# Optimization experiments

Hardware: AMD Instinct MI355X
Metric: run time of the kernel (lower is better)

The kernel has to match this reference:

```python
import jax, jax.numpy as jnp
import numpy as np
import math

B_, M_, T_, E_ = 4, 4, 128, 512
S_ = M_ * T_
H_ = 2048
NE, NS, TOPK, NHEAD = 8, 2, 2, 4
P_, GRUH, AK, AV = 128, 128, 64, 64


def _ln(x, s, b, eps=1e-5):
    mu = x.mean(-1, keepdims=True)
    var = x.var(-1, keepdims=True)
    return (x - mu) / jnp.sqrt(var + eps) * s + b


def _gru(x, Wih, bih, Whh, bhh):
    # x: [N, T, D] -> [N, T, GRUH]; torch nn.GRU cell equations
    Hh = Whh.shape[1]
    def step(h, xt):
        gi = xt @ Wih.T + bih
        gh = h @ Whh.T + bhh
        ir, iz, inn = jnp.split(gi, 3, axis=-1)
        hr, hz, hn = jnp.split(gh, 3, axis=-1)
        r = jax.nn.sigmoid(ir + hr)
        z = jax.nn.sigmoid(iz + hz)
        n = jnp.tanh(inn + r * hn)
        h = (1.0 - z) * n + z * h
        return h, h
    h0 = jnp.zeros((x.shape[0], Hh), x.dtype)
    _, hs = jax.lax.scan(step, h0, jnp.swapaxes(x, 0, 1))
    return jnp.swapaxes(hs, 0, 1)


def _router_logits(x4, rU, rR, rS, Wtp, btp, Wq, bq, Wk, bk, Wv, bv,
                   gWih, gbih, gWhh, gbhh, mW1, mb1, mW2, mb2):
    B, M, T, E = x4.shape
    proc = jax.nn.relu(x4 @ Wtp + btp)                  # [B,M,T,P]
    q = proc @ Wq + bq                                   # [B,M,T,AK]
    Rp = jnp.transpose(rR, (0, 3, 1, 2))                 # [B,T,M,M]
    Sp = jnp.transpose(rS, (0, 3, 1, 2))
    others = np.array([[j for j in range(M) if j != m] for m in range(M)])  # [M,M-1]
    mi = np.arange(M)[:, None]
    feat = jnp.stack([Rp[:, :, mi, others], Sp[:, :, mi, others]], axis=-1)  # [B,T,M,M-1,2]
    keys = feat @ Wk + bk                                # [B,T,M,M-1,AK]
    vals = feat @ Wv + bv                                # [B,T,M,M-1,AV]
    sc = jnp.einsum('bmtk,btmok->bmto', q, keys) / math.sqrt(AK)
    ctx = jnp.einsum('bmto,btmov->bmtv', jax.nn.softmax(sc, -1), vals)  # [B,M,T,AV]
    gin = jnp.concatenate([rU[..., None], ctx], -1).reshape(B * M, T, 1 + AV)
    hs = _gru(gin, gWih, gbih, gWhh, gbhh).reshape(B, M, T, GRUH)
    comb = jnp.concatenate([proc, hs], -1)               # [B,M,T,P+GRUH]
    return jax.nn.relu(comb @ mW1 + mb1) @ mW2 + mb2     # [B,M,T,NE]


def _forward(x, rU, rR, rS, M, T, Wtp, btp, Wq, bq, Wk, bk, Wv, bv,
             gWih, gbih, gWhh, gbhh, mW1, mb1, mW2, mb2,
             sWq, sbq, sWk, sbk, sWv, sbv, sWo, sbo, sln1s, sln1b,
             sW1, sb1, sW2, sb2, sln2s, sln2b, fW1, fb1, fW2, fb2):
    B, S, E = x.shape
    x4 = x.reshape(B, M, T, E)
    logits = _router_logits(x4, rU, rR, rS, Wtp, btp, Wq, bq, Wk, bk, Wv, bv,
                            gWih, gbih, gWhh, gbhh, mW1, mb1, mW2, mb2)
    NT = B * S
    lf = logits.reshape(NT, NE)
    probs = jax.nn.softmax(lf, -1)
    vals, idx = jax.lax.top_k(lf, TOPK)
    tw = jax.nn.softmax(vals, -1)                        # renormalized top-k weights
    tok = x.reshape(NT, E)
    out = jnp.zeros((NT, E), x.dtype)
    hd = E // NHEAD
    for e in range(NE):
        w = jnp.sum(jnp.where(idx == e, tw, 0.0), -1)    # [NT] per-token weight for expert e
        if e < NS:
            # synergy expert: self-attention restricted to tokens routed here.
            # Sort routed tokens to the front (fixed capacity NT) and mask keys.
            valid = w > 0
            order = jnp.argsort(jnp.where(valid, 0, 1), stable=True)
            xg, vg = tok[order], valid[order]
            qh = (xg @ sWq[e] + sbq[e]).reshape(NT, NHEAD, hd)
            kh = (xg @ sWk[e] + sbk[e]).reshape(NT, NHEAD, hd)
            vh = (xg @ sWv[e] + sbv[e]).reshape(NT, NHEAD, hd)
            sc = jnp.einsum('nhd,mhd->hnm', qh, kh) / math.sqrt(hd)
            sc = jnp.where(vg[None, None, :], sc, -1e9)
            ao = jnp.einsum('hnm,mhd->nhd', jax.nn.softmax(sc, -1), vh).reshape(NT, E)
            ao = ao @ sWo[e] + sbo[e]
            h1 = _ln(xg + ao, sln1s[e], sln1b[e])
            ff = jax.nn.relu(h1 @ sW1[e] + sb1[e]) @ sW2[e] + sb2[e]
            y = _ln(h1 + ff, sln2s[e], sln2b[e])
            out = out.at[order].add(y * w[order][:, None])
        else:
            # FFN expert is pointwise -> dense compute weighted by w (w==0 elsewhere)
            f = e - NS
            y = jax.nn.relu(tok @ fW1[f] + fb1[f]) @ fW2[f] + fb2[f]
            out = out + y * w[:, None]
    return (out.reshape(B, S, E), probs.reshape(B, M, T, NE),
            idx.reshape(B, M, T, TOPK))


def setup_inputs() -> dict:
    key = jax.random.key(0)
    ks = iter(jax.random.split(key, 64))
    def rn(shape, s=0.02):
        return jax.random.normal(next(ks), shape, dtype=jnp.float32) * s
    Cm = (P_ + GRUH) // 2
    return {
        'x': jax.random.normal(next(ks), (B_, S_, E_), dtype=jnp.float32),
        'rU': jax.random.uniform(next(ks), (B_, M_, T_), dtype=jnp.float32),
        'rR': jax.random.uniform(next(ks), (B_, M_, M_, T_), dtype=jnp.float32),
        'rS': jax.random.uniform(next(ks), (B_, M_, M_, T_), dtype=jnp.float32),
        'M': M_, 'T': T_,
        'Wtp': rn((E_, P_)), 'btp': jnp.zeros((P_,)),
        'Wq': rn((P_, AK)), 'bq': jnp.zeros((AK,)),
        'Wk': rn((2, AK)), 'bk': jnp.zeros((AK,)),
        'Wv': rn((2, AV)), 'bv': jnp.zeros((AV,)),
        'gWih': rn((3 * GRUH, 1 + AV)), 'gbih': jnp.zeros((3 * GRUH,)),
        'gWhh': rn((3 * GRUH, GRUH)), 'gbhh': jnp.zeros((3 * GRUH,)),
        'mW1': rn((P_ + GRUH, Cm)), 'mb1': jnp.zeros((Cm,)),
        'mW2': rn((Cm, NE)), 'mb2': jnp.zeros((NE,)),
        'sWq': rn((NS, E_, E_)), 'sbq': jnp.zeros((NS, E_)),
        'sWk': rn((NS, E_, E_)), 'sbk': jnp.zeros((NS, E_)),
        'sWv': rn((NS, E_, E_)), 'sbv': jnp.zeros((NS, E_)),
        'sWo': rn((NS, E_, E_)), 'sbo': jnp.zeros((NS, E_)),
        'sln1s': jnp.ones((NS, E_)), 'sln1b': jnp.zeros((NS, E_)),
        'sW1': rn((NS, E_, H_)), 'sb1': jnp.zeros((NS, H_)),
        'sW2': rn((NS, H_, E_)), 'sb2': jnp.zeros((NS, E_)),
        'sln2s': jnp.ones((NS, E_)), 'sln2b': jnp.zeros((NS, E_)),
        'fW1': rn((NE - NS, E_, H_)), 'fb1': jnp.zeros((NE - NS, H_)),
        'fW2': rn((NE - NS, H_, E_)), 'fb2': jnp.zeros((NE - NS, E_)),
    }


def reference(x, rU, rR, rS, M, T, Wtp, btp, Wq, bq, Wk, bk, Wv, bv,
              gWih, gbih, gWhh, gbhh, mW1, mb1, mW2, mb2,
              sWq, sbq, sWk, sbk, sWv, sbv, sWo, sbo, sln1s, sln1b,
              sW1, sb1, sW2, sb2, sln2s, sln2b, fW1, fb1, fW2, fb2):
    return _forward(x, rU, rR, rS, M, T, Wtp, btp, Wq, bq, Wk, bk, Wv, bv,
                    gWih, gbih, gWhh, gbhh, mW1, mb1, mW2, mb2,
                    sWq, sbq, sWk, sbk, sWv, sbv, sWo, sbo, sln1s, sln1b,
                    sW1, sb1, sW2, sb2, sln2s, sln2b, fW1, fb1, fW2, fb2)
```

## Files before the change

kernel.cpp:

```cpp
#include <hip/hip_runtime.h>
#include <math.h>

#define Bc 4
#define Mc 4
#define Tc 128
#define Ec 512
#define Hc 2048
#define NEc 8
#define NSc 2
#define NHEADc 4
#define Pc 128
#define GRUHc 128
#define AKc 64
#define AVc 64
#define NTc 2048
#define HDc 128

typedef __bf16 bfv8 __attribute__((ext_vector_type(8)));
typedef float f32x4 __attribute__((ext_vector_type(4)));
typedef float f32v16 __attribute__((ext_vector_type(16)));

__global__ __launch_bounds__(256)
void zero_k(float* __restrict__ out, int* __restrict__ cnt)
{
    int i = blockIdx.x * 256 + threadIdx.x;
    float4* o4 = (float4*)out;
    if (i < (NTc * Ec) / 4) o4[i] = make_float4(0.f, 0.f, 0.f, 0.f);
    if (i < NEc) cnt[i] = 0;
}

struct CJob { const float* src; __bf16* dst; };
struct CJobs8 { CJob j[8]; };

__global__ __launch_bounds__(256)
void convT_k(CJobs8 jobs, int K, int N)
{
    CJob J = jobs.j[blockIdx.z];
    __shared__ float t[32][33];
    int bx = blockIdx.x * 32;
    int by = blockIdx.y * 32;
    int tx = threadIdx.x & 31, ty = threadIdx.x >> 5;
#pragma unroll
    for (int i = 0; i < 4; ++i) {
        int k = by + ty + i * 8, n = bx + tx;
        t[ty + i * 8][tx] = (k < K && n < N) ? J.src[(size_t)k * N + n] : 0.f;
    }
    __syncthreads();
#pragma unroll
    for (int i = 0; i < 4; ++i) {
        int n = bx + ty + i * 8, k = by + tx;
        if (n < N && k < K) J.dst[(size_t)n * K + k] = (__bf16)t[tx][ty + i * 8];
    }
}

__global__ __launch_bounds__(256)
void gemm_k(const float* __restrict__ A, int lda,
            const float* __restrict__ B, int ldb,
            const float* __restrict__ bias,
            float* __restrict__ C, int ldc,
            int M, int N, int K, int relu)
{
    int tm = blockIdx.x * 64, tn = blockIdx.y * 64;
    if (tm >= M || tn >= N) return;
    __shared__ float As[16][68];
    __shared__ float Bs[16][68];
    int tid = threadIdx.x;
    int tx = tid & 15, ty = tid >> 4;
    float acc[4][4] = {};
    int arow = tid >> 2;
    int ak0  = (tid & 3) * 4;
    int bk   = tid >> 4;
    int bc0  = (tid & 15) * 4;
    int grA = tm + arow;
    const float* Arow = (grA < M) ? (A + (size_t)grA * lda) : nullptr;

    for (int k0 = 0; k0 < K; k0 += 16) {
#pragma unroll
        for (int u = 0; u < 4; ++u) {
            int k = k0 + ak0 + u;
            As[ak0 + u][arow] = (Arow && k < K) ? Arow[k] : 0.f;
        }
        int kb = k0 + bk;
#pragma unroll
        for (int u = 0; u < 4; ++u) {
            int n2 = tn + bc0 + u;
            Bs[bk][bc0 + u] = (kb < K && n2 < N) ? B[(size_t)kb * ldb + n2] : 0.f;
        }
        __syncthreads();
#pragma unroll
        for (int kk = 0; kk < 16; ++kk) {
            float a0 = As[kk][ty * 4 + 0], a1 = As[kk][ty * 4 + 1];
            float a2 = As[kk][ty * 4 + 2], a3 = As[kk][ty * 4 + 3];
            float b0 = Bs[kk][tx * 4 + 0], b1 = Bs[kk][tx * 4 + 1];
            float b2 = Bs[kk][tx * 4 + 2], b3 = Bs[kk][tx * 4 + 3];
            acc[0][0] += a0 * b0; acc[0][1] += a0 * b1; acc[0][2] += a0 * b2; acc[0][3] += a0 * b3;
            acc[1][0] += a1 * b0; acc[1][1] += a1 * b1; acc[1][2] += a1 * b2; acc[1][3] += a1 * b3;
            acc[2][0] += a2 * b0; acc[2][1] += a2 * b1; acc[2][2] += a2 * b2; acc[2][3] += a2 * b3;
            acc[3][0] += a3 * b0; acc[3][1] += a3 * b1; acc[3][2] += a3 * b2; acc[3][3] += a3 * b3;
        }
        __syncthreads();
    }
#pragma unroll
    for (int i = 0; i < 4; ++i) {
        int gr = tm + ty * 4 + i;
        if (gr >= M) continue;
#pragma unroll
        for (int j = 0; j < 4; ++j) {
            int gc = tn + tx * 4 + j;
            if (gc >= N) continue;
            float v = acc[i][j] + (bias ? bias[gc] : 0.f);
            if (relu) v = fmaxf(v, 0.f);
            C[(size_t)gr * ldc + gc] = v;
        }
    }
}

struct GJob {
    const void* A;
    const void* B;
    const float* bias;
    void* C;
    const int* Mptr;
    const int* gatherA;
    float* scatterOut;
    const int* scatterList;
    const float* wvec;
    int ldc;
    int flags;
};
struct GJobs6 { GJob j[6]; };

#define LDA_S 40
template<int AMODE>
__global__ __launch_bounds__(256)
void gemm_batch_k(GJobs6 jobs, int lda, int ldb, int N, int K)
{
    GJob J = jobs.j[blockIdx.z];
    int M = *J.Mptr;
    int tm = blockIdx.x * 128, tn = blockIdx.y * 128;
    if (tm >= M || tn >= N) return;

    __shared__ __bf16 As[128 * LDA_S];
    __shared__ __bf16 Bs[128 * LDA_S];
    int tid = threadIdx.x, lane = tid & 63, wvi = tid >> 6;
    int wm = (wvi & 1) * 64, wn = (wvi >> 1) * 64;
    f32x4 acc[4][4] = {};

    int ar = tid >> 1, ah = (tid & 1) * 16;
    const float*  Apf = nullptr;
    const __bf16* Apb = nullptr;
    if (tm + ar < M) {
        int g = J.gatherA ? J.gatherA[tm + ar] : (tm + ar);
        if (AMODE == 0) Apf = (const float*)J.A + (size_t)g * lda;
        else            Apb = (const __bf16*)J.A + (size_t)g * lda;
    }
    const __bf16* Bp = ((tn + ar) < N) ? ((const __bf16*)J.B + (size_t)(tn + ar) * ldb)
                                       : nullptr;

    float fa[16];
    bfv8 ra0, ra1, rb0, rb1;

    auto LOADA = [&](int k0) {
        int kb = k0 + ah;
        if (AMODE == 0) {
            if (Apf) {
                const float4* p = (const float4*)(Apf + kb);
                float4 x0 = p[0], x1 = p[1], x2 = p[2], x3 = p[3];
                fa[0]=x0.x; fa[1]=x0.y; fa[2]=x0.z; fa[3]=x0.w;
                fa[4]=x1.x; fa[5]=x1.y; fa[6]=x1.z; fa[7]=x1.w;
                fa[8]=x2.x; fa[9]=x2.y; fa[10]=x2.z; fa[11]=x2.w;
                fa[12]=x3.x; fa[13]=x3.y; fa[14]=x3.z; fa[15]=x3.w;
            } else {
#pragma unroll
                for (int i = 0; i < 16; ++i) fa[i] = 0.f;
            }
        } else {
            if (Apb) {
                ra0 = *(const bfv8*)(Apb + kb);
                ra1 = *(const bfv8*)(Apb + kb + 8);
            } else {
#pragma unroll
                for (int i = 0; i < 8; ++i) { ra0[i] = (__bf16)0.f; ra1[i] = (__bf16)0.f; }
            }
        }
    };
    auto LOADB = [&](int k0) {
        int kb = k0 + ah;
        if (Bp) {
            rb0 = *(const bfv8*)(Bp + kb);
            rb1 = *(const bfv8*)(Bp + kb + 8);
        } else {
#pragma unroll
            for (int i = 0; i < 8; ++i) { rb0[i] = (__bf16)0.f; rb1[i] = (__bf16)0.f; }
        }
    };

    int KT = K / 32;
    LOADA(0);
    LOADB(0);

    for (int kt = 0; kt < KT; ++kt) {
        __syncthreads();
        if (AMODE == 0) {
            bfv8 p0, p1;
#pragma unroll
            for (int i = 0; i < 8; ++i) { p0[i] = (__bf16)fa[i]; p1[i] = (__bf16)fa[8 + i]; }
            *(bfv8*)(As + ar * LDA_S + ah) = p0;
            *(bfv8*)(As + ar * LDA_S + ah + 8) = p1;
        } else {
            *(bfv8*)(As + ar * LDA_S + ah) = ra0;
            *(bfv8*)(As + ar * LDA_S + ah + 8) = ra1;
        }
        *(bfv8*)(Bs + ar * LDA_S + ah) = rb0;
        *(bfv8*)(Bs + ar * LDA_S + ah + 8) = rb1;
        __syncthreads();
        if (kt + 1 < KT) {
            LOADA((kt + 1) * 32);
            LOADB((kt + 1) * 32);
        }
        {
            int fr = lane & 15, quad = lane >> 4;
            bfv8 af[4], bfr[4];
            const __bf16* Ab = As + quad * 8 + fr * LDA_S;
            const __bf16* Bb2 = Bs + quad * 8 + fr * LDA_S;
#pragma unroll
            for (int t2 = 0; t2 < 4; ++t2) {
                af[t2]  = *(const bfv8*)(Ab + (wm + t2 * 16) * LDA_S);
                bfr[t2] = *(const bfv8*)(Bb2 + (wn + t2 * 16) * LDA_S);
            }
#pragma unroll
            for (int i = 0; i < 4; ++i)
#pragma unroll
                for (int j = 0; j < 4; ++j)
                    acc[i][j] = __builtin_amdgcn_mfma_f32_16x16x32_bf16(af[i], bfr[j], acc[i][j], 0, 0, 0);
        }
    }

    int col = lane & 15, rq = (lane >> 4) * 4;
    int relu = J.flags & 1, storeT = J.flags & 2, storeBf = J.flags & 4;
#pragma unroll
    for (int ti = 0; ti < 4; ++ti) {
#pragma unroll
        for (int tj = 0; tj < 4; ++tj) {
#pragma unroll
            for (int r = 0; r < 4; ++r) {
                int gm = tm + wm + ti * 16 + rq + r;
                int gn = tn + wn + tj * 16 + col;
                if (gm < M && gn < N) {
                    float v = acc[ti][tj][r] + (J.bias ? J.bias[gn] : 0.f);
                    if (relu) v = fmaxf(v, 0.f);
                    if (J.scatterOut) {
                        int g = J.scatterList[gm];
                        atomicAdd(&J.scatterOut[(size_t)g * Ec + gn], v * J.wvec[(size_t)g * NEc]);
                    } else if (storeT) {
                        ((float*)J.C)[(size_t)gn * J.ldc + gm] = v;
                    } else if (storeBf) {
                        ((__bf16*)J.C)[(size_t)gm * J.ldc + gn] = (__bf16)v;
                    } else {
                        ((float*)J.C)[(size_t)gm * J.ldc + gn] = v;
                    }
                }
            }
        }
    }
}

__global__ __launch_bounds__(256)
void flash_k(const float* __restrict__ QbB, const float* __restrict__ KbB,
             const float* __restrict__ VtB, float* __restrict__ AOB,
             const int* __restrict__ cntB)
{
    int e = blockIdx.z;
    const float* Qb = QbB + (size_t)e * NTc * Ec;
    const float* Kb = KbB + (size_t)e * NTc * Ec;
    const float* Vt = VtB + (size_t)e * NTc * Ec;
    float* AO = AOB + (size_t)e * NTc * Ec;
    int nv = cntB[e];
    int r0 = blockIdx.x * 64;
    if (r0 >= nv) return;
    int h = blockIdx.y;
    const int QS = 136, VS = 72;
    __shared__ __bf16 Ql[64 * 136];
    __shared__ __bf16 Kl[64 * 136];
    __shared__ __bf16 Vl[128 * 72];
    __shared__ __bf16 Pl[64 * 72];
    int tid = threadIdx.x, lane = tid & 63, wv = tid >> 6;
    int fr = lane & 15, quad = lane >> 4;

    {
        int qr = tid >> 2, c0 = (tid & 3) * 32;
        const float* src = Qb + (size_t)(r0 + qr) * Ec + h * HDc + c0;
        __bf16* dst = Ql + qr * QS + c0;
        bool ok = (r0 + qr) < nv;
#pragma unroll
        for (int u = 0; u < 8; ++u) {
            float4 v = ok ? ((const float4*)src)[u] : make_float4(0.f, 0.f, 0.f, 0.f);
            dst[u*4+0] = (__bf16)v.x; dst[u*4+1] = (__bf16)v.y;
            dst[u*4+2] = (__bf16)v.z; dst[u*4+3] = (__bf16)v.w;
        }
    }

    f32x4 accO[8];
#pragma unroll
    for (int j = 0; j < 8; ++j) accO[j] = (f32x4){0.f, 0.f, 0.f, 0.f};
    float mrow[4] = {-1e30f, -1e30f, -1e30f, -1e30f};
    float lrow[4] = {0.f, 0.f, 0.f, 0.f};
    const float invsq = 0.08838834764831845f;

    for (int j0 = 0; j0 < nv; j0 += 64) {
        __syncthreads();
        {
            int kr = tid >> 2, c0 = (tid & 3) * 32;
            const float* src = Kb + (size_t)(j0 + kr) * Ec + h * HDc + c0;
            __bf16* dst = Kl + kr * QS + c0;
            bool ok = (j0 + kr) < nv;
#pragma unroll
            for (int u = 0; u < 8; ++u) {
                float4 v = ok ? ((const float4*)src)[u] : make_float4(0.f, 0.f, 0.f, 0.f);
                dst[u*4+0] = (__bf16)v.x; dst[u*4+1] = (__bf16)v.y;
                dst[u*4+2] = (__bf16)v.z; dst[u*4+3] = (__bf16)v.w;
            }
        }
        {
            int dr = tid >> 1, c0 = (tid & 1) * 32;
            const float* src = Vt + (size_t)(h * HDc + dr) * NTc + j0 + c0;
            __bf16* dst = Vl + dr * VS + c0;
            int rem = nv - (j0 + c0);
            if (rem >= 32) {
#pragma unroll
                for (int u = 0; u < 8; ++u) {
                    float4 v = ((const float4*)src)[u];
                    dst[u*4+0] = (__bf16)v.x; dst[u*4+1] = (__bf16)v.y;
                    dst[u*4+2] = (__bf16)v.z; dst[u*4+3] = (__bf16)v.w;
                }
            } else {
                for (int u = 0; u < 32; ++u)
                    dst[u] = (u < rem) ? (__bf16)src[u] : (__bf16)0.f;
            }
        }
        __syncthreads();

        f32x4 sc[4] = {};
#pragma unroll
        for (int ks = 0; ks < 4; ++ks) {
            bfv8 aq = *(const bfv8*)(Ql + (wv * 16 + fr) * QS + ks * 32 + quad * 8);
#pragma unroll
            for (int tj = 0; tj < 4; ++tj) {
                bfv8 bk8 = *(const bfv8*)(Kl + (tj * 16 + fr) * QS + ks * 32 + quad * 8);
                sc[tj] = __builtin_amdgcn_mfma_f32_16x16x32_bf16(aq, bk8, sc[tj], 0, 0, 0);
            }
        }

        float alpha[4];
#pragma unroll
        for (int r = 0; r < 4; ++r) {
            float sv[4];
            float mx = -1e30f;
#pragma unroll
            for (int tj = 0; tj < 4; ++tj) {
                float s = sc[tj][r] * invsq;
                bool valid = (j0 + tj * 16 + fr) < nv;
                s = valid ? s : -1e30f;
                sv[tj] = s;
                mx = fmaxf(mx, s);
            }
#pragma unroll
            for (int off = 1; off < 16; off <<= 1)
                mx = fmaxf(mx, __shfl_xor(mx, off, 64));
            float mn = fmaxf(mrow[r], mx);
            alpha[r] = expf(mrow[r] - mn);
            float ps = 0.f;
#pragma unroll
            for (int tj = 0; tj < 4; ++tj) {
                bool valid = (j0 + tj * 16 + fr) < nv;
                float p = valid ? expf(sv[tj] - mn) : 0.f;
                Pl[(wv * 16 + quad * 4 + r) * VS + tj * 16 + fr] = (__bf16)p;
                ps += p;
            }
#pragma unroll
            for (int off = 1; off < 16; off <<= 1)
                ps += __shfl_xor(ps, off, 64);
            lrow[r] = lrow[r] * alpha[r] + ps;
            mrow[r] = mn;
        }
#pragma unroll
        for (int tj = 0; tj < 8; ++tj)
#pragma unroll
            for (int r = 0; r < 4; ++r)
                accO[tj][r] *= alpha[r];
#pragma unroll
        for (int ks = 0; ks < 2; ++ks) {
            bfv8 ap = *(const bfv8*)(Pl + (wv * 16 + fr) * VS + ks * 32 + quad * 8);
#pragma unroll
            for (int tj = 0; tj < 8; ++tj) {
                bfv8 bv8 = *(const bfv8*)(Vl + (tj * 16 + fr) * VS + ks * 32 + quad * 8);
                accO[tj] = __builtin_amdgcn_mfma_f32_16x16x32_bf16(ap, bv8, accO[tj], 0, 0, 0);
            }
        }
    }

#pragma unroll
    for (int r = 0; r < 4; ++r) {
        int row = r0 + wv * 16 + quad * 4 + r;
        if (row < nv) {
            float invl = 1.f / lrow[r];
#pragma unroll
            for (int tj = 0; tj < 8; ++tj)
                AO[(size_t)row * Ec + h * HDc + tj * 16 + fr] = accO[tj][r] * invl;
        }
    }
}

__global__ __launch_bounds__(256)
void router_ctx_k(const float* __restrict__ q4, const float* __restrict__ rR,
                  const float* __restrict__ rS,
                  const float* __restrict__ Wk, const float* __restrict__ bk,
                  const float* __restrict__ Wv, const float* __restrict__ bv,
                  float* __restrict__ ctx)
{
    int tid = threadIdx.x;
    int lane = tid & 63;
    int n = blockIdx.x * 4 + (tid >> 6);
    int m = (n >> 7) & 3, t = n & 127, b = n >> 9;
    float q = q4[(size_t)n * AKc + lane];
    float sc[3], rv[3], sv[3];
#pragma unroll
    for (int o = 0; o < 3; ++o) {
        int oth = o + (o >= m ? 1 : 0);
        float r = rR[(((size_t)(b * Mc + m)) * Mc + oth) * Tc + t];
        float s_ = rS[(((size_t)(b * Mc + m)) * Mc + oth) * Tc + t];
        rv[o] = r; sv[o] = s_;
        float key = r * Wk[lane] + s_ * Wk[64 + lane] + bk[lane];
        float p = q * key;
#pragma unroll
        for (int off = 32; off; off >>= 1) p += __shfl_xor(p, off, 64);
        sc[o] = p * 0.125f;
    }
    float mx = fmaxf(sc[0], fmaxf(sc[1], sc[2]));
    float e0 = expf(sc[0] - mx), e1 = expf(sc[1] - mx), e2 = expf(sc[2] - mx);
    float inv = 1.f / (e0 + e1 + e2);
    float p0 = e0 * inv, p1 = e1 * inv, p2 = e2 * inv;
    float v0 = rv[0] * Wv[lane] + sv[0] * Wv[64 + lane] + bv[lane];
    float v1 = rv[1] * Wv[lane] + sv[1] * Wv[64 + lane] + bv[lane];
    float v2 = rv[2] * Wv[lane] + sv[2] * Wv[64 + lane] + bv[lane];
    ctx[(size_t)n * AVc + lane] = p0 * v0 + p1 * v1 + p2 * v2;
}

__global__ __launch_bounds__(256)
void gi_k(const float* __restrict__ rU, const float* __restrict__ ctx,
          const float* __restrict__ gWih, const float* __restrict__ gbih,
          float* __restrict__ gi)
{
    int idx = blockIdx.x * 256 + threadIdx.x;
    int g = idx % 384, nt = idx / 384;
    const float* Wr = gWih + (size_t)g * 65;
    float a = gbih[g] + rU[nt] * Wr[0];
    const float* c = ctx + (size_t)nt * AVc;
#pragma unroll
    for (int d = 0; d < 64; ++d) a += c[d] * Wr[1 + d];
    gi[(size_t)nt * 384 + g] = a;
}

__global__ __launch_bounds__(384, 1)
void gru_scan_k(const float* __restrict__ gi, const float* __restrict__ gWhh,
                const float* __restrict__ gbhh, float* __restrict__ hs)
{
    int seq = blockIdx.x, g = threadIdx.x;
    __shared__ float h[128];
    __shared__ float gh[384];
    const f32v16* wp = (const f32v16*)(gWhh + (size_t)g * 128);
    f32v16 w0 = wp[0], w1 = wp[1], w2 = wp[2], w3 = wp[3];
    f32v16 w4 = wp[4], w5 = wp[5], w6 = wp[6], w7 = wp[7];
    float bh = gbhh[g];
    if (g < 128) h[g] = 0.f;
    float g0 = 0.f, g1 = 0.f, g2 = 0.f;
    if (g < 128) {
        const float* gr = gi + (size_t)seq * 128 * 384;
        g0 = gr[g]; g1 = gr[128 + g]; g2 = gr[256 + g];
    }
    __syncthreads();
    for (int t = 0; t < 128; ++t) {
        float a0 = 0.f, a1 = 0.f, a2 = 0.f, a3 = 0.f;
#define GRU_STEP16(W, B) { \
        float4 x0 = *(const float4*)&h[B];      float4 x1 = *(const float4*)&h[(B) + 4]; \
        float4 x2 = *(const float4*)&h[(B) + 8]; float4 x3 = *(const float4*)&h[(B) + 12]; \
        a0 += x0.x * W[0];  a1 += x0.y * W[1];  a2 += x0.z * W[2];  a3 += x0.w * W[3]; \
        a0 += x1.x * W[4];  a1 += x1.y * W[5];  a2 += x1.z * W[6];  a3 += x1.w * W[7]; \
        a0 += x2.x * W[8];  a1 += x2.y * W[9];  a2 += x2.z * W[10]; a3 += x2.w * W[11]; \
        a0 += x3.x * W[12]; a1 += x3.y * W[13]; a2 += x3.z * W[14]; a3 += x3.w * W[15]; }
        GRU_STEP16(w0, 0)   GRU_STEP16(w1, 16)  GRU_STEP16(w2, 32)  GRU_STEP16(w3, 48)
        GRU_STEP16(w4, 64)  GRU_STEP16(w5, 80)  GRU_STEP16(w6, 96)  GRU_STEP16(w7, 112)
#undef GRU_STEP16
        gh[g] = bh + (a0 + a1) + (a2 + a3);
        __syncthreads();
        if (g < 128) {
            float r = 1.f / (1.f + expf(-(g0 + gh[g])));
            float z = 1.f / (1.f + expf(-(g1 + gh[128 + g])));
            float nn = tanhf(g2 + r * gh[256 + g]);
            float hn = (1.f - z) * nn + z * h[g];
            hs[((size_t)seq * 128 + t) * 128 + g] = hn;
            h[g] = hn;
            if (t + 1 < 128) {
                const float* gr = gi + ((size_t)seq * 128 + t + 1) * 384;
                g0 = gr[g]; g1 = gr[128 + g]; g2 = gr[256 + g];
            }
        }
        __syncthreads();
    }
}

__global__ __launch_bounds__(128)
void mlp_route_k(const float* __restrict__ proc, const float* __restrict__ hs,
                 const float* __restrict__ mW1, const float* __restrict__ mb1,
                 const float* __restrict__ mW2, const float* __restrict__ mb2,
                 float* __restrict__ probsOut, float* __restrict__ idxOut,
                 float* __restrict__ w)
{
    int n = blockIdx.x, tid = threadIdx.x;
    __shared__ float comb[256], tmp[128], lg[8];
    comb[tid] = proc[(size_t)n * 128 + tid];
    comb[128 + tid] = hs[(size_t)n * 128 + tid];
    __syncthreads();
    float a = mb1[tid];
#pragma unroll 8
    for (int d = 0; d < 256; ++d) a += comb[d] * mW1[(size_t)d * 128 + tid];
    tmp[tid] = fmaxf(a, 0.f);
    __syncthreads();
    if (tid < 8) {
        float l = mb2[tid];
        for (int d = 0; d < 128; ++d) l += tmp[d] * mW2[(size_t)d * 8 + tid];
        lg[tid] = l;
    }
    __syncthreads();
    if (tid == 0) {
        float mx = lg[0];
        for (int e = 1; e < 8; ++e) mx = fmaxf(mx, lg[e]);
        float p[8], s = 0.f;
        for (int e = 0; e < 8; ++e) { p[e] = expf(lg[e] - mx); s += p[e]; }
        float inv = 1.f / s;
        for (int e = 0; e < 8; ++e) probsOut[(size_t)n * 8 + e] = p[e] * inv;
        int a0 = 0; float v0 = lg[0];
        for (int e = 1; e < 8; ++e) if (lg[e] > v0) { v0 = lg[e]; a0 = e; }
        int a1 = -1; float v1 = -1e30f;
        for (int e = 0; e < 8; ++e) if (e != a0 && lg[e] > v1) { v1 = lg[e]; a1 = e; }
        float e1 = expf(v1 - v0);
        float t0 = 1.f / (1.f + e1), t1 = e1 / (1.f + e1);
        idxOut[(size_t)n * 2 + 0] = (float)a0;
        idxOut[(size_t)n * 2 + 1] = (float)a1;
        for (int e = 0; e < 8; ++e) w[(size_t)n * 8 + e] = 0.f;
        w[(size_t)n * 8 + a0] = t0;
        w[(size_t)n * 8 + a1] = t1;
    }
}

__global__ __launch_bounds__(256)
void compact_k(const float* __restrict__ w, int* __restrict__ cnt,
               int* __restrict__ list)
{
    int n = blockIdx.x * 256 + threadIdx.x;
    if (n >= NTc) return;
    for (int e = 0; e < NEc; ++e)
        if (w[(size_t)n * 8 + e] > 0.f) {
            int p = atomicAdd(&cnt[e], 1);
            list[e * NTc + p] = n;
        }
}

__global__ __launch_bounds__(256)
void ln1_k(const float* __restrict__ x, const int* __restrict__ listB,
           const float* __restrict__ addB, const float* __restrict__ sB,
           const float* __restrict__ bB, float* __restrict__ outB,
           const int* __restrict__ cntB)
{
    int e = blockIdx.y;
    int i = blockIdx.x;
    if (i >= cntB[e]) return;
    const int* list = listB + e * NTc;
    const float* add = addB + (size_t)e * NTc * Ec;
    const float* s = sB + e * Ec;
    const float* b = bB + e * Ec;
    float* outRows = outB + (size_t)e * NTc * Ec;
    int tid = threadIdx.x;
    int g = list[i];
    float v0 = x[(size_t)g * Ec + tid] + add[(size_t)i * Ec + tid];
    float v1 = x[(size_t)g * Ec + 256 + tid] + add[(size_t)i * Ec + 256 + tid];
    __shared__ float red[256];
    __shared__ float bc;
    red[tid] = v0 + v1; __syncthreads();
    for (int st = 128; st > 0; st >>= 1) { if (tid < st) red[tid] += red[tid + st]; __syncthreads(); }
    if (tid == 0) bc = red[0] * (1.f / 512.f);
    __syncthreads();
    float mu = bc;
    float d0 = v0 - mu, d1 = v1 - mu;
    __syncthreads();
    red[tid] = d0 * d0 + d1 * d1; __syncthreads();
    for (int st = 128; st > 0; st >>= 1) { if (tid < st) red[tid] += red[tid + st]; __syncthreads(); }
    if (tid == 0) bc = rsqrtf(red[0] * (1.f / 512.f) + 1e-5f);
    __syncthreads();
    float inv = bc;
    outRows[(size_t)i * Ec + tid] = d0 * inv * s[tid] + b[tid];
    outRows[(size_t)i * Ec + 256 + tid] = d1 * inv * s[256 + tid] + b[256 + tid];
}

__global__ __launch_bounds__(256)
void ln2_scatter_k(const float* __restrict__ H1B, const float* __restrict__ YB,
                   const float* __restrict__ sB, const float* __restrict__ bB,
                   float* __restrict__ out, const int* __restrict__ listB,
                   const int* __restrict__ cntB, const float* __restrict__ wB)
{
    int e = blockIdx.y;
    int i = blockIdx.x;
    if (i >= cntB[e]) return;
    const int* list = listB + e * NTc;
    const float* H1 = H1B + (size_t)e * NTc * Ec;
    const float* Y = YB + (size_t)e * NTc * Ec;
    const float* s = sB + e * Ec;
    const float* b = bB + e * Ec;
    const float* wvec = wB + e;
    int tid = threadIdx.x;
    int g = list[i];
    float v0 = H1[(size_t)i * Ec + tid] + Y[(size_t)i * Ec + tid];
    float v1 = H1[(size_t)i * Ec + 256 + tid] + Y[(size_t)i * Ec + 256 + tid];
    __shared__ float red[256];
    __shared__ float bc;
    red[tid] = v0 + v1; __syncthreads();
    for (int st = 128; st > 0; st >>= 1) { if (tid < st) red[tid] += red[tid + st]; __syncthreads(); }
    if (tid == 0) bc = red[0] * (1.f / 512.f);
    __syncthreads();
    float mu = bc;
    float d0 = v0 - mu, d1 = v1 - mu;
    __syncthreads();
    red[tid] = d0 * d0 + d1 * d1; __syncthreads();
    for (int st = 128; st > 0; st >>= 1) { if (tid < st) red[tid] += red[tid + st]; __syncthreads(); }
    if (tid == 0) bc = rsqrtf(red[0] * (1.f / 512.f) + 1e-5f);
    __syncthreads();
    float inv = bc;
    float wv = wvec[(size_t)g * 8];
    atomicAdd(&out[(size_t)g * Ec + tid], (d0 * inv * s[tid] + b[tid]) * wv);
    atomicAdd(&out[(size_t)g * Ec + 256 + tid], (d1 * inv * s[256 + tid] + b[256 + tid]) * wv);
}

extern "C" void kernel_launch(void* const* d_in, const int* in_sizes, int n_in,
                              void* d_out, int out_size, void* d_ws, size_t ws_size,
                              hipStream_t stream)
{
    const float* x    = (const float*)d_in[0];
    const float* rU   = (const float*)d_in[1];
    const float* rR   = (const float*)d_in[2];
    const float* rS   = (const float*)d_in[3];
    const float* Wtp  = (const float*)d_in[6];
    const float* btp  = (const float*)d_in[7];
    const float* Wq   = (const float*)d_in[8];
    const float* bq   = (const float*)d_in[9];
    const float* Wk   = (const float*)d_in[10];
    const float* bk   = (const float*)d_in[11];
    const float* Wv   = (const float*)d_in[12];
    const float* bv   = (const float*)d_in[13];
    const float* gWih = (const float*)d_in[14];
    const float* gbih = (const float*)d_in[15];
    const float* gWhh = (const float*)d_in[16];
    const float* gbhh = (const float*)d_in[17];
    const float* mW1  = (const float*)d_in[18];
    const float* mb1  = (const float*)d_in[19];
    const float* mW2  = (const float*)d_in[20];
    const float* mb2  = (const float*)d_in[21];
    const float* sWq  = (const float*)d_in[22];
    const float* sbq  = (const float*)d_in[23];
    const float* sWk  = (const float*)d_in[24];
    const float* sbk  = (const float*)d_in[25];
    const float* sWv  = (const float*)d_in[26];
    const float* sbv  = (const float*)d_in[27];
    const float* sWo  = (const float*)d_in[28];
    const float* sbo  = (const float*)d_in[29];
    const float* sln1s = (const float*)d_in[30];
    const float* sln1b = (const float*)d_in[31];
    const float* sW1  = (const float*)d_in[32];
    const float* sb1  = (const float*)d_in[33];
    const float* sW2  = (const float*)d_in[34];
    const float* sb2  = (const float*)d_in[35];
    const float* sln2s = (const float*)d_in[36];
    const float* sln2b = (const float*)d_in[37];
    const float* fW1  = (const float*)d_in[38];
    const float* fb1  = (const float*)d_in[39];
    const float* fW2  = (const float*)d_in[40];
    const float* fb2  = (const float*)d_in[41];

    float* out      = (float*)d_out;
    float* probsOut = out + (size_t)NTc * Ec;
    float* idxOut   = probsOut + (size_t)NTc * NEc;

    int*   cnt  = (int*)d_ws;
    int*   list = cnt + 64;
    float* w    = (float*)d_ws + 64 + NEc * NTc;
    __bf16* WB = (__bf16*)(w + NTc * NEc);
    auto QKVO_T = [&](int e, int i) { return WB + ((size_t)(e * 4 + i)) * 262144; };
    __bf16* sW1T = WB + 8 * 262144;
    __bf16* sW2T = sW1T + 2 * 1048576;
    __bf16* fW1T = sW2T + 2 * 1048576;
    __bf16* fW2T = fW1T + 3 * 1048576;
    float* act = (float*)(fW2T + 3 * 1048576);
    float* QbB = act;
    float* KbB = act + 2 * 1048576;
    float* VtB = act + 4 * 1048576;
    float* AOB = act + 6 * 1048576;
    float* H1B = act + 8 * 1048576;
    float* PRJB = QbB;
    float* YbB  = KbB;
    __bf16* FF1syn = (__bf16*)VtB;
    __bf16* FF1ffn = (__bf16*)act;
    float* proc = act;
    float* q4   = act + 262144;
    float* ctx  = act + 393216;
    float* gi   = act + 524288;
    float* hs   = act + 1310720;

    zero_k<<<1024, 256, 0, stream>>>(out, cnt);

    gemm_k<<<dim3(32, 2), 256, 0, stream>>>(x, Ec, Wtp, Pc, btp, proc, Pc, NTc, Pc, Ec, 1);
    gemm_k<<<dim3(32, 1), 256, 0, stream>>>(proc, Pc, Wq, AKc, bq, q4, AKc, NTc, AKc, Pc, 0);
    router_ctx_k<<<512, 256, 0, stream>>>(q4, rR, rS, Wk, bk, Wv, bv, ctx);
    gi_k<<<3072, 256, 0, stream>>>(rU, ctx, gWih, gbih, gi);
    gru_scan_k<<<16, 384, 0, stream>>>(gi, gWhh, gbhh, hs);
    mlp_route_k<<<2048, 128, 0, stream>>>(proc, hs, mW1, mb1, mW2, mb2,
                                          probsOut, idxOut, w);
    compact_k<<<8, 256, 0, stream>>>(w, cnt, list);

    GJob JZ = {};

    {
        CJobs8 cq = {};
        for (int e = 0; e < 2; ++e) {
            cq.j[e * 4 + 0] = { sWq + (size_t)e * Ec * Ec, QKVO_T(e, 0) };
            cq.j[e * 4 + 1] = { sWk + (size_t)e * Ec * Ec, QKVO_T(e, 1) };
            cq.j[e * 4 + 2] = { sWv + (size_t)e * Ec * Ec, QKVO_T(e, 2) };
            cq.j[e * 4 + 3] = { sWo + (size_t)e * Ec * Ec, QKVO_T(e, 3) };
        }
        convT_k<<<dim3(16, 16, 8), 256, 0, stream>>>(cq, Ec, Ec);
        CJobs8 c1 = {};
        c1.j[0] = { sW1, sW1T };
        c1.j[1] = { sW1 + (size_t)Ec * Hc, sW1T + 1048576 };
        convT_k<<<dim3(64, 16, 2), 256, 0, stream>>>(c1, Ec, Hc);
        CJobs8 c2 = {};
        c2.j[0] = { sW2, sW2T };
        c2.j[1] = { sW2 + (size_t)Hc * Ec, sW2T + 1048576 };
        convT_k<<<dim3(16, 64, 2), 256, 0, stream>>>(c2, Hc, Ec);
    }

    {
        GJobs6 js = {};
        for (int e = 0; e < 2; ++e) {
            GJob jq = JZ;
            jq.A = x; jq.Mptr = cnt + e; jq.gatherA = list + e * NTc;
            jq.B = QKVO_T(e, 0); jq.bias = sbq + e * Ec;
            jq.C = QbB + (size_t)e * NTc * Ec; jq.ldc = Ec; jq.flags = 0;
            GJob jk = jq; jk.B = QKVO_T(e, 1); jk.bias = sbk + e * Ec;
            jk.C = KbB + (size_t)e * NTc * Ec;
            GJob jv = jq; jv.B = QKVO_T(e, 2); jv.bias = sbv + e * Ec;
            jv.C = VtB + (size_t)e * NTc * Ec; jv.ldc = NTc; jv.flags = 2;
            js.j[e * 3 + 0] = jq; js.j[e * 3 + 1] = jk; js.j[e * 3 + 2] = jv;
        }
        gemm_batch_k<0><<<dim3(16, 4, 6), 256, 0, stream>>>(js, Ec, Ec, Ec, Ec);
    }

    flash_k<<<dim3(32, 4, 2), 256, 0, stream>>>(QbB, KbB, VtB, AOB, cnt);

    {
        GJobs6 js = {};
        for (int e = 0; e < 2; ++e) {
            GJob jo = JZ;
            jo.A = AOB + (size_t)e * NTc * Ec; jo.Mptr = cnt + e;
            jo.B = QKVO_T(e, 3); jo.bias = sbo + e * Ec;
            jo.C = PRJB + (size_t)e * NTc * Ec; jo.ldc = Ec;
            js.j[e] = jo;
        }
        gemm_batch_k<0><<<dim3(16, 4, 2), 256, 0, stream>>>(js, Ec, Ec, Ec, Ec);
    }

    ln1_k<<<dim3(2048, 2), 256, 0, stream>>>(x, list, PRJB, sln1s, sln1b, H1B, cnt);

    {
        GJobs6 js = {};
        for (int e = 0; e < 2; ++e) {
            GJob j1 = JZ;
            j1.A = H1B + (size_t)e * NTc * Ec; j1.Mptr = cnt + e;
            j1.B = sW1T + (size_t)e * 1048576; j1.bias = sb1 + (size_t)e * Hc;
            j1.C = FF1syn + (size_t)e * NTc * Hc; j1.ldc = Hc; j1.flags = 1 | 4;
            js.j[e] = j1;
        }
        gemm_batch_k<0><<<dim3(16, 16, 2), 256, 0, stream>>>(js, Ec, Ec, Hc, Ec);
    }

    {
        GJobs6 js = {};
        for (int e = 0; e < 2; ++e) {
            GJob j2 = JZ;
            j2.A = FF1syn + (size_t)e * NTc * Hc; j2.Mptr = cnt + e;
            j2.B = sW2T + (size_t)e * 1048576; j2.bias = sb2 + (size_t)e * Ec;
            j2.C = YbB + (size_t)e * NTc * Ec; j2.ldc = Ec;
            js.j[e] = j2;
        }
        gemm_batch_k<1><<<dim3(16, 4, 2), 256, 0, stream>>>(js, Hc, Hc, Ec, Hc);
    }

    ln2_scatter_k<<<dim3(2048, 2), 256, 0, stream>>>(H1B, YbB, sln2s, sln2b,
                                                     out, list, cnt, w);

    for (int rnd = 0; rnd < 2; ++rnd) {
        int f0 = rnd * 3;
        {
            CJobs8 a = {};
            for (int u = 0; u < 3; ++u)
                a.j[u] = { fW1 + (size_t)(f0 + u) * Ec * Hc, fW1T + (size_t)u * 1048576 };
            convT_k<<<dim3(64, 16, 3), 256, 0, stream>>>(a, Ec, Hc);
            CJobs8 b = {};
            for (int u = 0; u < 3; ++u)
                b.j[u] = { fW2 + (size_t)(f0 + u) * Hc * Ec, fW2T + (size_t)u * 1048576 };
            convT_k<<<dim3(16, 64, 3), 256, 0, stream>>>(b, Hc, Ec);
        }
        {
            GJobs6 js = {};
            for (int u = 0; u < 3; ++u) {
                int f = f0 + u, e = f + NSc;
                GJob j1 = JZ;
                j1.A = x; j1.Mptr = cnt + e; j1.gatherA = list + e * NTc;
                j1.B = fW1T + (size_t)u * 1048576; j1.bias = fb1 + (size_t)f * Hc;
                j1.C = FF1ffn + (size_t)u * NTc * Hc; j1.ldc = Hc; j1.flags = 1 | 4;
                js.j[u] = j1;
            }
            gemm_batch_k<0><<<dim3(16, 16, 3), 256, 0, stream>>>(js, Ec, Ec, Hc, Ec);
        }
        {
            GJobs6 js = {};
            for (int u = 0; u < 3; ++u) {
                int f = f0 + u, e = f + NSc;
                GJob j2 = JZ;
                j2.A = FF1ffn + (size_t)u * NTc * Hc; j2.Mptr = cnt + e;
                j2.B = fW2T + (size_t)u * 1048576; j2.bias = fb2 + (size_t)f * Ec;
                j2.scatterOut = out; j2.scatterList = list + e * NTc;
                j2.wvec = w + e; j2.ldc = Ec;
                js.j[u] = j2;
            }
            gemm_batch_k<1><<<dim3(16, 4, 3), 256, 0, stream>>>(js, Hc, Hc, Ec, Hc);
        }
    }
}
```

Measured before the change: 1.039 ms.

## Add split-K to batched GEMM, hoist FFN weight transposes, pin GRU weights in registers

Adds split-K support to the batched GEMM: blockIdx.y now carries both an N tile and a K chunk, and bias is added only by the first chunk. The scatter FF2 GEMM for the routed FFN experts is split four ways along K, with partial results combined by its existing atomicAdd scatter, to raise block count and occupancy on a K=2048 GEMM. The FFN weight transposes for all six experts are merged into one pair of launches ahead of the loop, using extra workspace, so two launch pairs become one. The GRU scan kernel changes its occupancy hint and adds an empty asm barrier to keep recurrent weights in VGPRs. Split-K adds more atomic traffic to the output.

```diff
diff --git a/kernel.cpp b/kernel.cpp
--- a/kernel.cpp
+++ b/kernel.cpp
@@ -133,12 +133,19 @@
 #define LDA_S 40
 template<int AMODE>
 __global__ __launch_bounds__(256)
-void gemm_batch_k(GJobs6 jobs, int lda, int ldb, int N, int K)
+void gemm_batch_k(GJobs6 jobs, int lda, int ldb, int N, int K,
+                  int nTilesY, int kIters)
 {
     GJob J = jobs.j[blockIdx.z];
     int M = *J.Mptr;
-    int tm = blockIdx.x * 128, tn = blockIdx.y * 128;
+    int by = blockIdx.y;
+    int ny = by % nTilesY, ko = by / nTilesY;
+    int tm = blockIdx.x * 128, tn = ny * 128;
     if (tm >= M || tn >= N) return;
+    int KT = K / 32;
+    int kt0 = ko * kIters;
+    int ktE = kt0 + kIters; if (ktE > KT) ktE = KT;
+    if (kt0 >= KT) return;
 
     __shared__ __bf16 As[128 * LDA_S];
     __shared__ __bf16 Bs[128 * LDA_S];
@@ -195,11 +202,10 @@
         }
     };
 
-    int KT = K / 32;
-    LOADA(0);
-    LOADB(0);
-
-    for (int kt = 0; kt < KT; ++kt) {
+    LOADA(kt0 * 32);
+    LOADB(kt0 * 32);
+
+    for (int kt = kt0; kt < ktE; ++kt) {
         __syncthreads();
         if (AMODE == 0) {
             bfv8 p0, p1;
@@ -214,7 +220,7 @@
         *(bfv8*)(Bs + ar * LDA_S + ah) = rb0;
         *(bfv8*)(Bs + ar * LDA_S + ah + 8) = rb1;
         __syncthreads();
-        if (kt + 1 < KT) {
+        if (kt + 1 < ktE) {
             LOADA((kt + 1) * 32);
             LOADB((kt + 1) * 32);
         }
@@ -238,6 +244,7 @@
 
     int col = lane & 15, rq = (lane >> 4) * 4;
     int relu = J.flags & 1, storeT = J.flags & 2, storeBf = J.flags & 4;
+    int addBias = (J.bias != nullptr) && (ko == 0);
 #pragma unroll
     for (int ti = 0; ti < 4; ++ti) {
 #pragma unroll
@@ -247,7 +254,7 @@
                 int gm = tm + wm + ti * 16 + rq + r;
                 int gn = tn + wn + tj * 16 + col;
                 if (gm < M && gn < N) {
-                    float v = acc[ti][tj][r] + (J.bias ? J.bias[gn] : 0.f);
+                    float v = acc[ti][tj][r] + (addBias ? J.bias[gn] : 0.f);
                     if (relu) v = fmaxf(v, 0.f);
                     if (J.scatterOut) {
                         int g = J.scatterList[gm];
@@ -461,7 +468,7 @@
     gi[(size_t)nt * 384 + g] = a;
 }
 
-__global__ __launch_bounds__(384, 1)
+__global__ __launch_bounds__(384) __attribute__((amdgpu_waves_per_eu(2, 2)))
 void gru_scan_k(const float* __restrict__ gi, const float* __restrict__ gWhh,
                 const float* __restrict__ gbhh, float* __restrict__ hs)
 {
@@ -471,6 +478,8 @@
     const f32v16* wp = (const f32v16*)(gWhh + (size_t)g * 128);
     f32v16 w0 = wp[0], w1 = wp[1], w2 = wp[2], w3 = wp[3];
     f32v16 w4 = wp[4], w5 = wp[5], w6 = wp[6], w7 = wp[7];
+    asm volatile("" : "+v"(w0), "+v"(w1), "+v"(w2), "+v"(w3),
+                      "+v"(w4), "+v"(w5), "+v"(w6), "+v"(w7));
     float bh = gbhh[g];
     if (g < 128) h[g] = 0.f;
     float g0 = 0.f, g1 = 0.f, g2 = 0.f;
@@ -708,6 +717,8 @@
     float* YbB  = KbB;
     __bf16* FF1syn = (__bf16*)VtB;
     __bf16* FF1ffn = (__bf16*)act;
+    __bf16* fW1T2 = FF1ffn + (size_t)3 * NTc * Hc;
+    __bf16* fW2T2 = fW1T2 + 3 * 1048576;
     float* proc = act;
     float* q4   = act + 262144;
     float* ctx  = act + 393216;
@@ -759,7 +770,7 @@
             jv.C = VtB + (size_t)e * NTc * Ec; jv.ldc = NTc; jv.flags = 2;
             js.j[e * 3 + 0] = jq; js.j[e * 3 + 1] = jk; js.j[e * 3 + 2] = jv;
         }
-        gemm_batch_k<0><<<dim3(16, 4, 6), 256, 0, stream>>>(js, Ec, Ec, Ec, Ec);
+        gemm_batch_k<0><<<dim3(16, 4, 6), 256, 0, stream>>>(js, Ec, Ec, Ec, Ec, 4, 16);
     }
 
     flash_k<<<dim3(32, 4, 2), 256, 0, stream>>>(QbB, KbB, VtB, AOB, cnt);
@@ -773,7 +784,7 @@
             jo.C = PRJB + (size_t)e * NTc * Ec; jo.ldc = Ec;
             js.j[e] = jo;
         }
-        gemm_batch_k<0><<<dim3(16, 4, 2), 256, 0, stream>>>(js, Ec, Ec, Ec, Ec);
+        gemm_batch_k<0><<<dim3(16, 4, 2), 256, 0, stream>>>(js, Ec, Ec, Ec, Ec, 4, 16);
     }
 
     ln1_k<<<dim3(2048, 2), 256, 0, stream>>>(x, list, PRJB, sln1s, sln1b, H1B, cnt);
@@ -787,7 +798,7 @@
             j1.C = FF1syn + (size_t)e * NTc * Hc; j1.ldc = Hc; j1.flags = 1 | 4;
             js.j[e] = j1;
         }
-        gemm_batch_k<0><<<dim3(16, 16, 2), 256, 0, stream>>>(js, Ec, Ec, Hc, Ec);
+        gemm_batch_k<0><<<dim3(16, 16, 2), 256, 0, stream>>>(js, Ec, Ec, Hc, Ec, 16, 16);
     }
 
     {
@@ -799,35 +810,42 @@
             j2.C = YbB + (size_t)e * NTc * Ec; j2.ldc = Ec;
             js.j[e] = j2;
         }
-        gemm_batch_k<1><<<dim3(16, 4, 2), 256, 0, stream>>>(js, Hc, Hc, Ec, Hc);
+        gemm_batch_k<1><<<dim3(16, 4, 2), 256, 0, stream>>>(js, Hc, Hc, Ec, Hc, 4, 64);
     }
 
     ln2_scatter_k<<<dim3(2048, 2), 256, 0, stream>>>(H1B, YbB, sln2s, sln2b,
                                                      out, list, cnt, w);
 
+    {
+        CJobs8 a = {};
+        for (int u = 0; u < 6; ++u)
+            a.j[u] = { fW1 + (size_t)u * Ec * Hc,
+                       (u < 3 ? fW1T + (size_t)u * 1048576
+                              : fW1T2 + (size_t)(u - 3) * 1048576) };
+        convT_k<<<dim3(64, 16, 6), 256, 0, stream>>>(a, Ec, Hc);
+        CJobs8 b = {};
+        for (int u = 0; u < 6; ++u)
+            b.j[u] = { fW2 + (size_t)u * Hc * Ec,
+                       (u < 3 ? fW2T + (size_t)u * 1048576
+                              : fW2T2 + (size_t)(u - 3) * 1048576) };
+        convT_k<<<dim3(16, 64, 6), 256, 0, stream>>>(b, Hc, Ec);
+    }
+
     for (int rnd = 0; rnd < 2; ++rnd) {
         int f0 = rnd * 3;
-        {
-            CJobs8 a = {};
-            for (int u = 0; u < 3; ++u)
-                a.j[u] = { fW1 + (size_t)(f0 + u) * Ec * Hc, fW1T + (size_t)u * 1048576 };
-            convT_k<<<dim3(64, 16, 3), 256, 0, stream>>>(a, Ec, Hc);
-            CJobs8 b = {};
-            for (int u = 0; u < 3; ++u)
-                b.j[u] = { fW2 + (size_t)(f0 + u) * Hc * Ec, fW2T + (size_t)u * 1048576 };
-            convT_k<<<dim3(16, 64, 3), 256, 0, stream>>>(b, Hc, Ec);
-        }
+        __bf16* W1 = rnd == 0 ? fW1T : fW1T2;
+        __bf16* W2 = rnd == 0 ? fW2T : fW2T2;
         {
             GJobs6 js = {};
             for (int u = 0; u < 3; ++u) {
                 int f = f0 + u, e = f + NSc;
                 GJob j1 = JZ;
                 j1.A = x; j1.Mptr = cnt + e; j1.gatherA = list + e * NTc;
-                j1.B = fW1T + (size_t)u * 1048576; j1.bias = fb1 + (size_t)f * Hc;
+                j1.B = W1 + (size_t)u * 1048576; j1.bias = fb1 + (size_t)f * Hc;
                 j1.C = FF1ffn + (size_t)u * NTc * Hc; j1.ldc = Hc; j1.flags = 1 | 4;
                 js.j[u] = j1;
             }
-            gemm_batch_k<0><<<dim3(16, 16, 3), 256, 0, stream>>>(js, Ec, Ec, Hc, Ec);
+            gemm_batch_k<0><<<dim3(16, 16, 3), 256, 0, stream>>>(js, Ec, Ec, Hc, Ec, 16, 16);
         }
         {
             GJobs6 js = {};
@@ -835,12 +853,12 @@
                 int f = f0 + u, e = f + NSc;
                 GJob j2 = JZ;
                 j2.A = FF1ffn + (size_t)u * NTc * Hc; j2.Mptr = cnt + e;
-                j2.B = fW2T + (size_t)u * 1048576; j2.bias = fb2 + (size_t)f * Ec;
+                j2.B = W2 + (size_t)u * 1048576; j2.bias = fb2 + (size_t)f * Ec;
                 j2.scatterOut = out; j2.scatterList = list + e * NTc;
                 j2.wvec = w + e; j2.ldc = Ec;
                 js.j[u] = j2;
             }
-            gemm_batch_k<1><<<dim3(16, 4, 3), 256, 0, stream>>>(js, Hc, Hc, Ec, Hc);
-        }
-    }
-}
+            gemm_batch_k<1><<<dim3(16, 16, 3), 256, 0, stream>>>(js, Hc, Hc, Ec, Hc, 4, 16);
+        }
+    }
+}
```

Measured after the change: 985.6 us. -5.2%, faster.
